# Optimization experiments

Measured on AMD Instinct MI355X. Metric: run time of the kernel, lower is better.

## Reference

```python
import jax, jax.numpy as jnp
import numpy as np

B, C, H, W = 32, 512, 32, 32
C8 = C // 8


def setup_inputs() -> dict:
    key = jax.random.key(0)
    ks = jax.random.split(key, 10)
    s = 1.0 / np.sqrt(C)
    return {
        "x": jax.random.normal(ks[0], (B, C, H, W), dtype=jnp.float32),
        "hha": jax.random.normal(ks[1], (B, C, H, W), dtype=jnp.float32),
        "wq": jax.random.normal(ks[2], (C8, C), dtype=jnp.float32) * s,
        "bq": jax.random.normal(ks[3], (C8,), dtype=jnp.float32) * 0.01,
        "wk": jax.random.normal(ks[4], (C8, C), dtype=jnp.float32) * s,
        "bk": jax.random.normal(ks[5], (C8,), dtype=jnp.float32) * 0.01,
        "wv": jax.random.normal(ks[6], (C, C), dtype=jnp.float32) * s,
        "bv": jax.random.normal(ks[7], (C,), dtype=jnp.float32) * 0.01,
        "gamma": jax.random.normal(ks[8], (1,), dtype=jnp.float32) * 0.5,
    }


def reference(x, hha, wq, bq, wk, bk, wv, bv, gamma):
    b, c, h, w = x.shape
    hw = h * w
    # 1x1 convs == per-pixel channel matmuls
    q = (jnp.einsum('bchw,oc->bohw', x, wq) + bq[None, :, None, None]).reshape(b, -1, hw)
    k = (jnp.einsum('bchw,oc->bohw', x, wk) + bk[None, :, None, None]).reshape(b, -1, hw)
    v = (jnp.einsum('bchw,oc->bohw', x, wv) + bv[None, :, None, None]).reshape(b, c, hw)
    # energy[b, i, j] = q[b, :, i] . k[b, :, j]  (no 1/sqrt(d) scaling, as in source)
    energy = jnp.einsum('bci,bcj->bij', q, k)          # [B, HW, HW]
    attention = jax.nn.softmax(energy, axis=-1)
    # out = V @ attention^T : out[b, c, i] = sum_j v[b, c, j] * attention[b, i, j]
    out = jnp.einsum('bcj,bij->bci', v, attention).reshape(b, c, h, w)
    rgb_out = gamma * out + x
    hha_out = gamma * out + hha
    return (attention, rgb_out, hha_out)
```

## Files before the change

kernel.cpp:

```cpp
#include <hip/hip_runtime.h>

#define B_N   32
#define C_N   512
#define HW_N  1024
#define C8_N  64

typedef short bf16x8 __attribute__((ext_vector_type(8)));
typedef float f32x4  __attribute__((ext_vector_type(4)));

static __device__ __forceinline__ unsigned int bf16_bits(float a)
{
    unsigned int u = __float_as_uint(a);
    return (u + 0x7fffu + ((u >> 16) & 1u)) >> 16;
}

static __device__ __forceinline__ unsigned int pack2_bf16(float a, float b)
{
    return bf16_bits(a) | (bf16_bits(b) << 16);
}

__global__ __launch_bounds__(256) void xsplit_transpose_kernel(
    const float* __restrict__ x, unsigned int* __restrict__ xt)
{
    const int b   = blockIdx.z;
    const int c0  = blockIdx.y * 64;
    const int p0  = blockIdx.x * 64;
    const int tid = threadIdx.x;

    __shared__ unsigned int Ls[64][65];

    const float* xb = x + ((size_t)b * C_N + c0) * HW_N + p0;
    {
        const int c = tid >> 4;
        const int p = (tid & 15) * 4;
        #pragma unroll
        for (int s = 0; s < 4; ++s) {
            const float4 t = *(const float4*)(xb + (size_t)(c + 16 * s) * HW_N + p);
            const float v[4] = { t.x, t.y, t.z, t.w };
            #pragma unroll
            for (int j = 0; j < 4; ++j) {
                const unsigned int hi = bf16_bits(v[j]);
                const float hif = __uint_as_float(hi << 16);
                const unsigned int lo = bf16_bits(v[j] - hif);
                Ls[c + 16 * s][p + j] = (hi << 16) | lo;
            }
        }
    }
    __syncthreads();
    unsigned int* xo = xt + ((size_t)b * HW_N + p0) * C_N + c0;
    {
        const int p = tid >> 4;
        const int c = (tid & 15) * 4;
        #pragma unroll
        for (int s = 0; s < 4; ++s) {
            uint4 r;
            r.x = Ls[c + 0][p + 16 * s];
            r.y = Ls[c + 1][p + 16 * s];
            r.z = Ls[c + 2][p + 16 * s];
            r.w = Ls[c + 3][p + 16 * s];
            *(uint4*)(xo + (size_t)(p + 16 * s) * C_N + c) = r;
        }
    }
}

__global__ __launch_bounds__(256) void qkv_mfma_kernel(
    const unsigned int* __restrict__ xt,
    const float* __restrict__ wq, const float* __restrict__ bq,
    const float* __restrict__ wk, const float* __restrict__ bk,
    const float* __restrict__ wv, const float* __restrict__ bv,
    float* __restrict__ qk, unsigned short* __restrict__ vout)
{
    const int b    = blockIdx.z;
    const int by   = blockIdx.y;
    const int p0   = blockIdx.x * 128;
    const int tid  = threadIdx.x;
    const bool qkblk = (by == 0);

    __shared__ __align__(16) unsigned short AsHi[128 * 64];
    __shared__ __align__(16) unsigned short AsLo[128 * 64];
    __shared__ __align__(16) unsigned short BsHi[128 * 64];
    __shared__ __align__(16) unsigned short BsLo[128 * 64];

    const int sq = tid & 7;
    const int sr = tid >> 3;

    const int lane = tid & 63;
    const int wave = tid >> 6;
    const int wrow = (wave >> 1) * 64;
    const int wcol = (wave & 1) * 64;
    const int lrow = lane & 15;
    const int lk   = lane >> 4;

    const unsigned int* bt = xt + ((size_t)b * HW_N + p0) * C_N;

    f32x4 acc[4][4] = {};
    float4 ra[4][2];
    uint4  rb[4][2];

    auto wrowptr = [&](int r) -> const float* {
        if (qkblk) return (r < 64) ? (wq + (size_t)r * C_N)
                                   : (wk + (size_t)(r - 64) * C_N);
        return wv + (size_t)((by - 1) * 128 + r) * C_N;
    };

    auto load_tiles = [&](int k0) {
        #pragma unroll
        for (int s = 0; s < 4; ++s) {
            const int r = sr + 32 * s;
            const float* pa = wrowptr(r) + k0 + sq * 8;
            ra[s][0] = *(const float4*)(pa);
            ra[s][1] = *(const float4*)(pa + 4);
            const unsigned int* pb = bt + (size_t)r * C_N + k0 + sq * 8;
            rb[s][0] = *(const uint4*)(pb);
            rb[s][1] = *(const uint4*)(pb + 4);
        }
    };

    auto write_tiles = [&]() {
        #pragma unroll
        for (int s = 0; s < 4; ++s) {
            const int r  = sr + 32 * s;
            const int ch = sq ^ (r & 7);
            const float e[8] = { ra[s][0].x, ra[s][0].y, ra[s][0].z, ra[s][0].w,
                                 ra[s][1].x, ra[s][1].y, ra[s][1].z, ra[s][1].w };
            unsigned int h[8];
            #pragma unroll
            for (int j = 0; j < 8; ++j) h[j] = bf16_bits(e[j]);
            uint4 ah;
            ah.x = h[0] | (h[1] << 16); ah.y = h[2] | (h[3] << 16);
            ah.z = h[4] | (h[5] << 16); ah.w = h[6] | (h[7] << 16);
            *reinterpret_cast<uint4*>(&AsHi[r * 64 + ch * 8]) = ah;
            if (qkblk) {
                unsigned int l[8];
                #pragma unroll
                for (int j = 0; j < 8; ++j) {
                    const float hf = __uint_as_float(h[j] << 16);
                    l[j] = bf16_bits(e[j] - hf);
                }
                uint4 al;
                al.x = l[0] | (l[1] << 16); al.y = l[2] | (l[3] << 16);
                al.z = l[4] | (l[5] << 16); al.w = l[6] | (l[7] << 16);
                *reinterpret_cast<uint4*>(&AsLo[r * 64 + ch * 8]) = al;
            }
            const unsigned int q0[8] = { rb[s][0].x, rb[s][0].y, rb[s][0].z, rb[s][0].w,
                                         rb[s][1].x, rb[s][1].y, rb[s][1].z, rb[s][1].w };
            uint4 bh, bl;
            bh.x = (q0[0] >> 16) | (q0[1] & 0xffff0000u);
            bh.y = (q0[2] >> 16) | (q0[3] & 0xffff0000u);
            bh.z = (q0[4] >> 16) | (q0[5] & 0xffff0000u);
            bh.w = (q0[6] >> 16) | (q0[7] & 0xffff0000u);
            bl.x = (q0[0] & 0xffffu) | (q0[1] << 16);
            bl.y = (q0[2] & 0xffffu) | (q0[3] << 16);
            bl.z = (q0[4] & 0xffffu) | (q0[5] << 16);
            bl.w = (q0[6] & 0xffffu) | (q0[7] << 16);
            *reinterpret_cast<uint4*>(&BsHi[r * 64 + ch * 8]) = bh;
            *reinterpret_cast<uint4*>(&BsLo[r * 64 + ch * 8]) = bl;
        }
    };

    load_tiles(0);
    for (int kt = 0; kt < C_N / 64; ++kt) {
        __syncthreads();
        write_tiles();
        __syncthreads();
        if (kt + 1 < C_N / 64) load_tiles((kt + 1) * 64);

        #pragma unroll
        for (int kb = 0; kb < 2; ++kb) {
            bf16x8 bfh[4], bfl[4];
            #pragma unroll
            for (int n = 0; n < 4; ++n) {
                const int r  = wcol + n * 16 + lrow;
                const int ch = (kb * 4 + lk) ^ (lrow & 7);
                bfh[n] = *reinterpret_cast<const bf16x8*>(&BsHi[r * 64 + ch * 8]);
                bfl[n] = *reinterpret_cast<const bf16x8*>(&BsLo[r * 64 + ch * 8]);
            }
            #pragma unroll
            for (int m = 0; m < 4; ++m) {
                const int r  = wrow + m * 16 + lrow;
                const int ch = (kb * 4 + lk) ^ (lrow & 7);
                const bf16x8 ah = *reinterpret_cast<const bf16x8*>(&AsHi[r * 64 + ch * 8]);
                #pragma unroll
                for (int n = 0; n < 4; ++n) {
                    acc[m][n] = __builtin_amdgcn_mfma_f32_16x16x32_bf16(ah, bfh[n], acc[m][n], 0, 0, 0);
                    acc[m][n] = __builtin_amdgcn_mfma_f32_16x16x32_bf16(ah, bfl[n], acc[m][n], 0, 0, 0);
                }
                if (qkblk) {
                    const bf16x8 al = *reinterpret_cast<const bf16x8*>(&AsLo[r * 64 + ch * 8]);
                    #pragma unroll
                    for (int n = 0; n < 4; ++n)
                        acc[m][n] = __builtin_amdgcn_mfma_f32_16x16x32_bf16(al, bfh[n], acc[m][n], 0, 0, 0);
                }
            }
        }
    }

    #pragma unroll
    for (int m = 0; m < 4; ++m) {
        #pragma unroll
        for (int rr = 0; rr < 4; ++rr) {
            const int r = wrow + m * 16 + lk * 4 + rr;
            if (qkblk) {
                const float bi = (r < 64) ? bq[r] : bk[r - 64];
                float* dst = qk + ((size_t)b * 128 + r) * HW_N + p0 + wcol + lrow;
                #pragma unroll
                for (int n = 0; n < 4; ++n)
                    dst[n * 16] = acc[m][n][rr] + bi;
            } else {
                const int vr = (by - 1) * 128 + r;
                const float bi = bv[vr];
                unsigned short* dst = vout + ((size_t)b * C_N + vr) * HW_N + p0 + wcol + lrow;
                #pragma unroll
                for (int n = 0; n < 4; ++n)
                    dst[n * 16] = (unsigned short)bf16_bits(acc[m][n][rr] + bi);
            }
        }
    }
}

__global__ __launch_bounds__(256) void energy_kernel(
    const float* __restrict__ qkbuf, float* __restrict__ att)
{
    const int b   = blockIdx.z;
    const int i0  = blockIdx.y * 64;
    const int j0  = blockIdx.x * 64;
    const int tid = threadIdx.x;
    const int tx  = tid & 15;
    const int ty  = tid >> 4;

    const float* q = qkbuf + (size_t)b * 128 * HW_N;
    const float* k = q + (size_t)C8_N * HW_N;

    __shared__ float Qs[16][65];
    __shared__ float Ks[16][65];
    float acc[4][4] = {};

    for (int c0 = 0; c0 < C8_N; c0 += 16) {
        const int c = tid >> 4;
        const int u = (tid & 15) * 4;
        {
            const float4 t = *(const float4*)(q + (size_t)(c0 + c) * HW_N + i0 + u);
            Qs[c][u + 0] = t.x; Qs[c][u + 1] = t.y;
            Qs[c][u + 2] = t.z; Qs[c][u + 3] = t.w;
        }
        {
            const float4 t = *(const float4*)(k + (size_t)(c0 + c) * HW_N + j0 + u);
            Ks[c][u + 0] = t.x; Ks[c][u + 1] = t.y;
            Ks[c][u + 2] = t.z; Ks[c][u + 3] = t.w;
        }
        __syncthreads();
        #pragma unroll
        for (int cc = 0; cc < 16; ++cc) {
            float qi[4], kj[4];
            #pragma unroll
            for (int i = 0; i < 4; ++i) qi[i] = Qs[cc][ty * 4 + i];
            #pragma unroll
            for (int j = 0; j < 4; ++j) kj[j] = Ks[cc][tx * 4 + j];
            #pragma unroll
            for (int i = 0; i < 4; ++i)
                #pragma unroll
                for (int j = 0; j < 4; ++j)
                    acc[i][j] = fmaf(qi[i], kj[j], acc[i][j]);
        }
        __syncthreads();
    }

    #pragma unroll
    for (int i = 0; i < 4; ++i) {
        float4 r;
        r.x = acc[i][0]; r.y = acc[i][1]; r.z = acc[i][2]; r.w = acc[i][3];
        *(float4*)(att + ((size_t)b * HW_N + i0 + ty * 4 + i) * HW_N + j0 + tx * 4) = r;
    }
}

__global__ __launch_bounds__(256) void softmax_kernel(float* __restrict__ att)
{
    const size_t row = blockIdx.x;
    float* e = att + row * (size_t)HW_N;
    const int tid  = threadIdx.x;
    const int wv_  = tid >> 6;
    const int lane = tid & 63;

    float4 v = ((const float4*)e)[tid];

    float m = fmaxf(fmaxf(v.x, v.y), fmaxf(v.z, v.w));
    #pragma unroll
    for (int off = 32; off > 0; off >>= 1)
        m = fmaxf(m, __shfl_down(m, off, 64));
    __shared__ float red[4];
    if (lane == 0) red[wv_] = m;
    __syncthreads();
    m = fmaxf(fmaxf(red[0], red[1]), fmaxf(red[2], red[3]));
    __syncthreads();

    float4 ex;
    ex.x = __expf(v.x - m); ex.y = __expf(v.y - m);
    ex.z = __expf(v.z - m); ex.w = __expf(v.w - m);
    float s = ex.x + ex.y + ex.z + ex.w;
    #pragma unroll
    for (int off = 32; off > 0; off >>= 1)
        s += __shfl_down(s, off, 64);
    if (lane == 0) red[wv_] = s;
    __syncthreads();
    s = red[0] + red[1] + red[2] + red[3];

    const float inv = 1.0f / s;
    ex.x *= inv; ex.y *= inv; ex.z *= inv; ex.w *= inv;
    ((float4*)e)[tid] = ex;
}

__global__ __launch_bounds__(256) void out_kernel(
    const unsigned short* __restrict__ vout, const float* __restrict__ att,
    const float* __restrict__ x, const float* __restrict__ hha,
    const float* __restrict__ gamma,
    float* __restrict__ rgb, float* __restrict__ hho)
{
    const int b   = blockIdx.z;
    const int c0  = blockIdx.y * 128;
    const int i0  = blockIdx.x * 128;
    const int tid = threadIdx.x;

    const unsigned short* vptr = vout + (size_t)(b * C_N + c0) * HW_N;
    const float* aptr = att + (size_t)b * HW_N * HW_N + (size_t)i0 * HW_N;

    __shared__ __align__(16) unsigned short Vs[128 * 64];
    __shared__ __align__(16) unsigned short Ps[128 * 64];

    const int sq = tid & 7;
    const int sr = tid >> 3;

    const int lane = tid & 63;
    const int wave = tid >> 6;
    const int wrow = (wave >> 1) * 64;
    const int wcol = (wave & 1) * 64;
    const int lrow = lane & 15;
    const int lk   = lane >> 4;

    f32x4 acc[4][4] = {};
    uint4  ra[4];
    float4 rb[4][2];

    auto load_tiles = [&](int j0) {
        #pragma unroll
        for (int s = 0; s < 4; ++s) {
            ra[s] = *(const uint4*)(vptr + (size_t)(sr + 32 * s) * HW_N + j0 + sq * 8);
            const float* pb = aptr + (size_t)(sr + 32 * s) * HW_N + j0 + sq * 8;
            rb[s][0] = *(const float4*)(pb);
            rb[s][1] = *(const float4*)(pb + 4);
        }
    };

    auto write_tiles = [&]() {
        #pragma unroll
        for (int s = 0; s < 4; ++s) {
            const int r  = sr + 32 * s;
            const int ch = sq ^ (r & 7);
            *reinterpret_cast<uint4*>(&Vs[r * 64 + ch * 8]) = ra[s];
            uint4 wb;
            wb.x = pack2_bf16(rb[s][0].x, rb[s][0].y);
            wb.y = pack2_bf16(rb[s][0].z, rb[s][0].w);
            wb.z = pack2_bf16(rb[s][1].x, rb[s][1].y);
            wb.w = pack2_bf16(rb[s][1].z, rb[s][1].w);
            *reinterpret_cast<uint4*>(&Ps[r * 64 + ch * 8]) = wb;
        }
    };

    load_tiles(0);
    for (int jt = 0; jt < HW_N / 64; ++jt) {
        __syncthreads();
        write_tiles();
        __syncthreads();
        if (jt + 1 < HW_N / 64) load_tiles((jt + 1) * 64);

        #pragma unroll
        for (int kb = 0; kb < 2; ++kb) {
            bf16x8 af[4], bf[4];
            #pragma unroll
            for (int m = 0; m < 4; ++m) {
                const int r  = wrow + m * 16 + lrow;
                const int ch = (kb * 4 + lk) ^ (lrow & 7);
                af[m] = *reinterpret_cast<const bf16x8*>(&Vs[r * 64 + ch * 8]);
            }
            #pragma unroll
            for (int n = 0; n < 4; ++n) {
                const int r  = wcol + n * 16 + lrow;
                const int ch = (kb * 4 + lk) ^ (lrow & 7);
                bf[n] = *reinterpret_cast<const bf16x8*>(&Ps[r * 64 + ch * 8]);
            }
            #pragma unroll
            for (int m = 0; m < 4; ++m)
                #pragma unroll
                for (int n = 0; n < 4; ++n)
                    acc[m][n] = __builtin_amdgcn_mfma_f32_16x16x32_bf16(
                        af[m], bf[n], acc[m][n], 0, 0, 0);
        }
    }

    const float g    = gamma[0];
    const int   crow = c0 + wrow + lk * 4;
    const int   icol = i0 + wcol + lrow;
    #pragma unroll
    for (int m = 0; m < 4; ++m) {
        #pragma unroll
        for (int rr = 0; rr < 4; ++rr) {
            const int c = crow + m * 16 + rr;
            const size_t base = ((size_t)b * C_N + c) * HW_N + icol;
            #pragma unroll
            for (int n = 0; n < 4; ++n) {
                const float o  = acc[m][n][rr];
                const float xv = x[base + n * 16];
                const float hv = hha[base + n * 16];
                rgb[base + n * 16] = fmaf(g, o, xv);
                hho[base + n * 16] = fmaf(g, o, hv);
            }
        }
    }
}

extern "C" void kernel_launch(void* const* d_in, const int* in_sizes, int n_in,
                              void* d_out, int out_size, void* d_ws, size_t ws_size,
                              hipStream_t stream)
{
    const float* x     = (const float*)d_in[0];
    const float* hha   = (const float*)d_in[1];
    const float* wq    = (const float*)d_in[2];
    const float* bq    = (const float*)d_in[3];
    const float* wk    = (const float*)d_in[4];
    const float* bk    = (const float*)d_in[5];
    const float* wv    = (const float*)d_in[6];
    const float* bv    = (const float*)d_in[7];
    const float* gamma = (const float*)d_in[8];

    float* out = (float*)d_out;
    float* att = out;
    float* rgb = att + (size_t)B_N * HW_N * HW_N;
    float* hho = rgb + (size_t)B_N * C_N * HW_N;

    float*          qkbuf = (float*)d_ws;
    unsigned short* vbuf  = (unsigned short*)((float*)d_ws + (size_t)B_N * 128 * HW_N);

    unsigned int* xt = (unsigned int*)att;

    xsplit_transpose_kernel<<<dim3(HW_N / 64, C_N / 64, B_N), 256, 0, stream>>>(x, xt);
    qkv_mfma_kernel<<<dim3(HW_N / 128, 5, B_N), 256, 0, stream>>>(
        xt, wq, bq, wk, bk, wv, bv, qkbuf, vbuf);
    energy_kernel<<<dim3(HW_N / 64, HW_N / 64, B_N), 256, 0, stream>>>(qkbuf, att);
    softmax_kernel<<<dim3(B_N * HW_N), 256, 0, stream>>>(att);
    out_kernel<<<dim3(HW_N / 128, C_N / 128, B_N), 256, 0, stream>>>(
        vbuf, att, x, hha, gamma, rgb, hho);
}
```

Measured before the change: 721.5 us.

## Compute energy with split-bf16 MFMA after transposing Q/K to pixel-major

Replaces the scalar FP32 shared-memory energy GEMM with an MFMA kernel that represents Q and K as hi+lo bf16 pairs and uses three bf16 MFMAs per tile to keep near-FP32 accuracy. A new transpose kernel converts the Q/K buffer to a pixel-major packed hi/lo layout, and the tiles go into swizzled LDS. This removes the CUDA-core FMA cost of the 32x1024x1024x64 product but adds an extra kernel launch, a workspace buffer and a small precision loss from dropping the lo*lo term.

```diff
diff --git a/kernel.cpp b/kernel.cpp
--- a/kernel.cpp
+++ b/kernel.cpp
@@ -218,58 +218,148 @@
     }
 }
 
-__global__ __launch_bounds__(256) void energy_kernel(
-    const float* __restrict__ qkbuf, float* __restrict__ att)
+__global__ __launch_bounds__(256) void qkt_transpose_kernel(
+    const float* __restrict__ qk, unsigned int* __restrict__ qkT)
 {
     const int b   = blockIdx.z;
-    const int i0  = blockIdx.y * 64;
-    const int j0  = blockIdx.x * 64;
+    const int m0  = blockIdx.y * 64;
+    const int p0  = blockIdx.x * 64;
     const int tid = threadIdx.x;
-    const int tx  = tid & 15;
-    const int ty  = tid >> 4;
-
-    const float* q = qkbuf + (size_t)b * 128 * HW_N;
-    const float* k = q + (size_t)C8_N * HW_N;
-
-    __shared__ float Qs[16][65];
-    __shared__ float Ks[16][65];
-    float acc[4][4] = {};
-
-    for (int c0 = 0; c0 < C8_N; c0 += 16) {
-        const int c = tid >> 4;
-        const int u = (tid & 15) * 4;
+
+    __shared__ unsigned int Ls[64][65];
+
+    const float* src = qk + ((size_t)b * 128 + m0) * HW_N + p0;
+    {
+        const int m = tid >> 4;
+        const int p = (tid & 15) * 4;
+        #pragma unroll
+        for (int s = 0; s < 4; ++s) {
+            const float4 t = *(const float4*)(src + (size_t)(m + 16 * s) * HW_N + p);
+            const float v[4] = { t.x, t.y, t.z, t.w };
+            #pragma unroll
+            for (int j = 0; j < 4; ++j) {
+                const unsigned int hi = bf16_bits(v[j]);
+                const float hif = __uint_as_float(hi << 16);
+                const unsigned int lo = bf16_bits(v[j] - hif);
+                Ls[m + 16 * s][p + j] = (hi << 16) | lo;
+            }
+        }
+    }
+    __syncthreads();
+    unsigned int* dst = qkT + ((size_t)b * HW_N + p0) * 128 + m0;
+    {
+        const int p = tid >> 4;
+        const int m = (tid & 15) * 4;
+        #pragma unroll
+        for (int s = 0; s < 4; ++s) {
+            uint4 r;
+            r.x = Ls[m + 0][p + 16 * s];
+            r.y = Ls[m + 1][p + 16 * s];
+            r.z = Ls[m + 2][p + 16 * s];
+            r.w = Ls[m + 3][p + 16 * s];
+            *(uint4*)(dst + (size_t)(p + 16 * s) * 128 + m) = r;
+        }
+    }
+}
+
+__global__ __launch_bounds__(256) void energy_mfma_kernel(
+    const unsigned int* __restrict__ qkT, float* __restrict__ att)
+{
+    const int b   = blockIdx.z;
+    const int i0  = blockIdx.y * 128;
+    const int j0  = blockIdx.x * 128;
+    const int tid = threadIdx.x;
+
+    __shared__ __align__(16) unsigned short AsHi[128 * 64];
+    __shared__ __align__(16) unsigned short AsLo[128 * 64];
+    __shared__ __align__(16) unsigned short BsHi[128 * 64];
+    __shared__ __align__(16) unsigned short BsLo[128 * 64];
+
+    const int sq = tid & 7;
+    const int sr = tid >> 3;
+
+    const int lane = tid & 63;
+    const int wave = tid >> 6;
+    const int wrow = (wave >> 1) * 64;
+    const int wcol = (wave & 1) * 64;
+    const int lrow = lane & 15;
+    const int lk   = lane >> 4;
+
+    #pragma unroll
+    for (int s = 0; s < 4; ++s) {
+        const int r  = sr + 32 * s;
+        const int ch = sq ^ (r & 7);
         {
-            const float4 t = *(const float4*)(q + (size_t)(c0 + c) * HW_N + i0 + u);
-            Qs[c][u + 0] = t.x; Qs[c][u + 1] = t.y;
-            Qs[c][u + 2] = t.z; Qs[c][u + 3] = t.w;
+            const unsigned int* pa = qkT + ((size_t)b * HW_N + i0 + r) * 128 + sq * 8;
+            const uint4 u0 = *(const uint4*)(pa);
+            const uint4 u1 = *(const uint4*)(pa + 4);
+            uint4 h, l;
+            h.x = (u0.x >> 16) | (u0.y & 0xffff0000u);
+            h.y = (u0.z >> 16) | (u0.w & 0xffff0000u);
+            h.z = (u1.x >> 16) | (u1.y & 0xffff0000u);
+            h.w = (u1.z >> 16) | (u1.w & 0xffff0000u);
+            l.x = (u0.x & 0xffffu) | (u0.y << 16);
+            l.y = (u0.z & 0xffffu) | (u0.w << 16);
+            l.z = (u1.x & 0xffffu) | (u1.y << 16);
+            l.w = (u1.z & 0xffffu) | (u1.w << 16);
+            *reinterpret_cast<uint4*>(&AsHi[r * 64 + ch * 8]) = h;
+            *reinterpret_cast<uint4*>(&AsLo[r * 64 + ch * 8]) = l;
         }
         {
-            const float4 t = *(const float4*)(k + (size_t)(c0 + c) * HW_N + j0 + u);
-            Ks[c][u + 0] = t.x; Ks[c][u + 1] = t.y;
-            Ks[c][u + 2] = t.z; Ks[c][u + 3] = t.w;
-        }
-        __syncthreads();
-        #pragma unroll
-        for (int cc = 0; cc < 16; ++cc) {
-            float qi[4], kj[4];
-            #pragma unroll
-            for (int i = 0; i < 4; ++i) qi[i] = Qs[cc][ty * 4 + i];
-            #pragma unroll
-            for (int j = 0; j < 4; ++j) kj[j] = Ks[cc][tx * 4 + j];
-            #pragma unroll
-            for (int i = 0; i < 4; ++i)
-                #pragma unroll
-                for (int j = 0; j < 4; ++j)
-                    acc[i][j] = fmaf(qi[i], kj[j], acc[i][j]);
-        }
-        __syncthreads();
-    }
-
-    #pragma unroll
-    for (int i = 0; i < 4; ++i) {
-        float4 r;
-        r.x = acc[i][0]; r.y = acc[i][1]; r.z = acc[i][2]; r.w = acc[i][3];
-        *(float4*)(att + ((size_t)b * HW_N + i0 + ty * 4 + i) * HW_N + j0 + tx * 4) = r;
+            const unsigned int* pb = qkT + ((size_t)b * HW_N + j0 + r) * 128 + 64 + sq * 8;
+            const uint4 u0 = *(const uint4*)(pb);
+            const uint4 u1 = *(const uint4*)(pb + 4);
+            uint4 h, l;
+            h.x = (u0.x >> 16) | (u0.y & 0xffff0000u);
+            h.y = (u0.z >> 16) | (u0.w & 0xffff0000u);
+            h.z = (u1.x >> 16) | (u1.y & 0xffff0000u);
+            h.w = (u1.z >> 16) | (u1.w & 0xffff0000u);
+            l.x = (u0.x & 0xffffu) | (u0.y << 16);
+            l.y = (u0.z & 0xffffu) | (u0.w << 16);
+            l.z = (u1.x & 0xffffu) | (u1.y << 16);
+            l.w = (u1.z & 0xffffu) | (u1.w << 16);
+            *reinterpret_cast<uint4*>(&BsHi[r * 64 + ch * 8]) = h;
+            *reinterpret_cast<uint4*>(&BsLo[r * 64 + ch * 8]) = l;
+        }
+    }
+    __syncthreads();
+
+    f32x4 acc[4][4] = {};
+    #pragma unroll
+    for (int kb = 0; kb < 2; ++kb) {
+        bf16x8 bfh[4], bfl[4];
+        #pragma unroll
+        for (int n = 0; n < 4; ++n) {
+            const int r  = wcol + n * 16 + lrow;
+            const int ch = (kb * 4 + lk) ^ (lrow & 7);
+            bfh[n] = *reinterpret_cast<const bf16x8*>(&BsHi[r * 64 + ch * 8]);
+            bfl[n] = *reinterpret_cast<const bf16x8*>(&BsLo[r * 64 + ch * 8]);
+        }
+        #pragma unroll
+        for (int m = 0; m < 4; ++m) {
+            const int r  = wrow + m * 16 + lrow;
+            const int ch = (kb * 4 + lk) ^ (lrow & 7);
+            const bf16x8 ah = *reinterpret_cast<const bf16x8*>(&AsHi[r * 64 + ch * 8]);
+            const bf16x8 al = *reinterpret_cast<const bf16x8*>(&AsLo[r * 64 + ch * 8]);
+            #pragma unroll
+            for (int n = 0; n < 4; ++n) {
+                acc[m][n] = __builtin_amdgcn_mfma_f32_16x16x32_bf16(ah, bfh[n], acc[m][n], 0, 0, 0);
+                acc[m][n] = __builtin_amdgcn_mfma_f32_16x16x32_bf16(ah, bfl[n], acc[m][n], 0, 0, 0);
+                acc[m][n] = __builtin_amdgcn_mfma_f32_16x16x32_bf16(al, bfh[n], acc[m][n], 0, 0, 0);
+            }
+        }
+    }
+
+    #pragma unroll
+    for (int m = 0; m < 4; ++m) {
+        #pragma unroll
+        for (int rr = 0; rr < 4; ++rr) {
+            const int i = i0 + wrow + m * 16 + lk * 4 + rr;
+            float* dst = att + ((size_t)b * HW_N + i) * HW_N + j0 + wcol + lrow;
+            #pragma unroll
+            for (int n = 0; n < 4; ++n)
+                dst[n * 16] = acc[m][n][rr];
+        }
     }
 }
 
@@ -437,14 +527,16 @@
     float* hho = rgb + (size_t)B_N * C_N * HW_N;
 
     float*          qkbuf = (float*)d_ws;
-    unsigned short* vbuf  = (unsigned short*)((float*)d_ws + (size_t)B_N * 128 * HW_N);
+    unsigned short* vbuf  = (unsigned short*)(qkbuf + (size_t)B_N * 128 * HW_N);
+    unsigned int*   qkTb  = (unsigned int*)(vbuf + (size_t)B_N * C_N * HW_N);
 
     unsigned int* xt = (unsigned int*)att;
 
     xsplit_transpose_kernel<<<dim3(HW_N / 64, C_N / 64, B_N), 256, 0, stream>>>(x, xt);
     qkv_mfma_kernel<<<dim3(HW_N / 128, 5, B_N), 256, 0, stream>>>(
         xt, wq, bq, wk, bk, wv, bv, qkbuf, vbuf);
-    energy_kernel<<<dim3(HW_N / 64, HW_N / 64, B_N), 256, 0, stream>>>(qkbuf, att);
+    qkt_transpose_kernel<<<dim3(HW_N / 64, 2, B_N), 256, 0, stream>>>(qkbuf, qkTb);
+    energy_mfma_kernel<<<dim3(HW_N / 128, HW_N / 128, B_N), 256, 0, stream>>>(qkTb, att);
     softmax_kernel<<<dim3(B_N * HW_N), 256, 0, stream>>>(att);
     out_kernel<<<dim3(HW_N / 128, C_N / 128, B_N), 256, 0, stream>>>(
         vbuf, att, x, hha, gamma, rgb, hho);
```

Result: faster. 678.0 us (-6.0%).
